# Kernel tuning notes

Hardware: AMD Instinct MI355X
Metric: run time of the kernel (lower is better)

Reference implementation:

```python
import jax, jax.numpy as jnp
import numpy as np

N = 50000
E = 625000
D = 128

def setup_inputs() -> dict:
    key = jax.random.key(0)
    ks = jax.random.split(key, 8)
    scale = 1.0 / np.sqrt(D)
    return {
        "x": jax.random.normal(ks[0], (N, D), dtype=jnp.float32),
        "edge_index": jax.random.randint(ks[1], (2, E), 0, N, dtype=jnp.int64),
        "W1_l": jax.random.normal(ks[2], (D, D), dtype=jnp.float32) * scale,
        "b1_l": jnp.zeros((D,), dtype=jnp.float32),
        "W1_r": jax.random.normal(ks[3], (D, D), dtype=jnp.float32) * scale,
        "W2_l": jax.random.normal(ks[4], (D, D), dtype=jnp.float32) * scale,
        "b2_l": jnp.zeros((D,), dtype=jnp.float32),
        "W2_r": jax.random.normal(ks[5], (D, D), dtype=jnp.float32) * scale,
    }

def _sage_conv(x, edge_index, W_l, b_l, W_r):
    # PyG SAGEConv: out = lin_l(mean_{j in N(i)} x_j) + lin_r(x_i)
    src, dst = edge_index[0], edge_index[1]
    n = x.shape[0]
    msg = x[src]                                              # [E, D] gather
    summed = jax.ops.segment_sum(msg, dst, num_segments=n)    # [N, D] scatter-add
    cnt = jax.ops.segment_sum(jnp.ones((src.shape[0],), x.dtype), dst, num_segments=n)
    mean = summed / jnp.maximum(cnt, 1.0)[:, None]            # zero in-degree -> 0
    return mean @ W_l.T + b_l + x @ W_r.T

def reference(x, edge_index, W1_l, b1_l, W1_r, W2_l, b2_l, W2_r):
    h = _sage_conv(x, edge_index, W1_l, b1_l, W1_r)
    h = jax.nn.relu(h)
    # dropout is identity in eval mode
    out = _sage_conv(h, edge_index, W2_l, b2_l, W2_r)
    return out
```

## Files before the change

kernel.cpp:

```cpp
#include <hip/hip_runtime.h>

#define D 128
#define CAP 64
#define MPAD 136
#define NBIN 196
#define BINCAP 4096
#define EPB 4096

typedef __attribute__((ext_vector_type(8))) short bf16x8;
typedef __attribute__((ext_vector_type(4))) float f32x4v;
typedef __attribute__((ext_vector_type(8))) unsigned short ushort8v;

__device__ __forceinline__ unsigned short f2b(float f) {
    unsigned int u = __float_as_uint(f);
    unsigned int r = (u + 0x7FFFu + ((u >> 16) & 1u)) >> 16;
    return (unsigned short)r;
}
__device__ __forceinline__ float b2f(unsigned short s) {
    return __uint_as_float(((unsigned int)s) << 16);
}


__global__ __launch_bounds__(256)
void prep(const float* __restrict__ x, ushort* __restrict__ xb, int n4,
          const float* __restrict__ a, const float* __restrict__ b,
          const float* __restrict__ c, const float* __restrict__ d,
          ushort* __restrict__ oa, ushort* __restrict__ ob,
          ushort* __restrict__ oc, ushort* __restrict__ od,
          int* __restrict__ ccur, ushort* __restrict__ hb, int n) {
    int i = blockIdx.x * blockDim.x + threadIdx.x;
    if (i < n4) {
        float4 v = ((const float4*)x)[i];
        ushort4 o;
        o.x = f2b(v.x); o.y = f2b(v.y); o.z = f2b(v.z); o.w = f2b(v.w);
        ((ushort4*)xb)[i] = o;
    }
    if (i < 16384) {
        int which = i >> 12, j = i & 4095;
        const float* s = which == 0 ? a : which == 1 ? b : which == 2 ? c : d;
        ushort* o = which == 0 ? oa : which == 1 ? ob : which == 2 ? oc : od;
        float4 v = ((const float4*)s)[j];
        ushort4 u;
        u.x = f2b(v.x); u.y = f2b(v.y); u.z = f2b(v.z); u.w = f2b(v.w);
        ((ushort4*)o)[j] = u;
    }
    if (i < NBIN) ccur[i] = 0;
    if (i < D) { xb[(size_t)n * D + i] = 0; hb[(size_t)n * D + i] = 0; }
}


__global__ __launch_bounds__(256)
void coarse_bin(const int* __restrict__ src, const int* __restrict__ dst, int E,
                int* __restrict__ ccur, unsigned int* __restrict__ packed) {
    __shared__ int hist[256];
    __shared__ int base[256];
    const int t = threadIdx.x;
    hist[t] = 0;
    __syncthreads();
    const int e0 = blockIdx.x * EPB;
    int mybin[16];
    int myrank[16];
    unsigned int myval[16];
#pragma unroll
    for (int k = 0; k < 16; ++k) {
        int e = e0 + k * 256 + t;
        mybin[k] = -1;
        if (e < E) {
            int dd = dst[e];
            int ss = src[e];
            int bb = dd >> 8;
            mybin[k] = bb;
            myval[k] = (unsigned int)ss | ((unsigned int)dd << 16);
            myrank[k] = atomicAdd(&hist[bb], 1);
        }
    }
    __syncthreads();
    if (t < NBIN && hist[t] > 0) base[t] = atomicAdd(&ccur[t], hist[t]);
    __syncthreads();
#pragma unroll
    for (int k = 0; k < 16; ++k) {
        if (mybin[k] >= 0) {
            int pos = base[mybin[k]] + myrank[k];
            if (pos < BINCAP) packed[(size_t)mybin[k] * BINCAP + pos] = myval[k];
        }
    }
}


__global__ __launch_bounds__(256)
void fine_csr(const unsigned int* __restrict__ packed, const int* __restrict__ ccur,
              unsigned short* __restrict__ csr, int* __restrict__ cnt, int n) {
    __shared__ int fh[256];
    const int b = blockIdx.x;
    const int t = threadIdx.x;
    fh[t] = 0;
    __syncthreads();
    int cb = min(ccur[b], BINCAP);
    const unsigned int* __restrict__ seg = packed + (size_t)b * BINCAP;
    for (int e = t; e < cb; e += 256) {
        unsigned int v = seg[e];
        int dd = (int)(v >> 16);
        int ss = (int)(v & 0xffffu);
        int r = atomicAdd(&fh[dd & 255], 1);
        if (r < CAP) csr[(size_t)dd * CAP + r] = (unsigned short)ss;
    }
    __syncthreads();
    int node = b * 256 + t;
    if (node < n) cnt[node] = fh[t];
}


template <int LAYER2>
__global__ __launch_bounds__(512, 2)
void sage_fused(const ushort* __restrict__ feat,
                const unsigned short* __restrict__ csr, const int* __restrict__ cnt,
                const ushort* __restrict__ Wl, const ushort* __restrict__ Wr,
                const float* __restrict__ bias, void* __restrict__ outp, int n) {
    __shared__ ushort Ms[128 * MPAD];
    __shared__ ushort As[128 * 32];
    __shared__ ushort Bs[128 * 32];
    const int tid = threadIdx.x;
    const int node0 = blockIdx.x * 128;

    {
        const int wv = tid >> 6;
        const int quad = (tid >> 4) & 3;
        const int l16 = tid & 15;
        const size_t co = (size_t)l16 * 8;
#pragma unroll 1
        for (int it = 0; it < 4; ++it) {
            int local = it * 32 + wv * 4 + quad;
            int node = node0 + local;
            float a0 = 0.f, a1 = 0.f, a2 = 0.f, a3 = 0.f, a4 = 0.f, a5 = 0.f, a6 = 0.f, a7 = 0.f;
            float b0 = 0.f, b1 = 0.f, b2 = 0.f, b3 = 0.f, b4 = 0.f, b5 = 0.f, b6 = 0.f, b7 = 0.f;
            float ic = 0.f;
            if (node < n) {
                int c = min(cnt[node], CAP);
                ic = 1.0f / (float)max(c, 1);
                const unsigned short* __restrict__ seg = csr + (size_t)node * CAP;
#pragma unroll 1
                for (int e = 0; e < c; e += 8) {
                    ushort8v s8 = *(const ushort8v*)&seg[e];
                    int i0 = (e + 0 < c) ? (int)s8[0] : n;
                    int i1 = (e + 1 < c) ? (int)s8[1] : n;
                    int i2 = (e + 2 < c) ? (int)s8[2] : n;
                    int i3 = (e + 3 < c) ? (int)s8[3] : n;
                    int i4 = (e + 4 < c) ? (int)s8[4] : n;
                    int i5 = (e + 5 < c) ? (int)s8[5] : n;
                    int i6 = (e + 6 < c) ? (int)s8[6] : n;
                    int i7 = (e + 7 < c) ? (int)s8[7] : n;
                    ushort8v v0 = *(const ushort8v*)&feat[(size_t)i0 * D + co];
                    ushort8v v1 = *(const ushort8v*)&feat[(size_t)i1 * D + co];
                    ushort8v v2 = *(const ushort8v*)&feat[(size_t)i2 * D + co];
                    ushort8v v3 = *(const ushort8v*)&feat[(size_t)i3 * D + co];
                    ushort8v v4 = *(const ushort8v*)&feat[(size_t)i4 * D + co];
                    ushort8v v5 = *(const ushort8v*)&feat[(size_t)i5 * D + co];
                    ushort8v v6 = *(const ushort8v*)&feat[(size_t)i6 * D + co];
                    ushort8v v7 = *(const ushort8v*)&feat[(size_t)i7 * D + co];
                    a0 += b2f(v0[0]); a1 += b2f(v0[1]); a2 += b2f(v0[2]); a3 += b2f(v0[3]);
                    a4 += b2f(v0[4]); a5 += b2f(v0[5]); a6 += b2f(v0[6]); a7 += b2f(v0[7]);
                    b0 += b2f(v1[0]); b1 += b2f(v1[1]); b2 += b2f(v1[2]); b3 += b2f(v1[3]);
                    b4 += b2f(v1[4]); b5 += b2f(v1[5]); b6 += b2f(v1[6]); b7 += b2f(v1[7]);
                    a0 += b2f(v2[0]); a1 += b2f(v2[1]); a2 += b2f(v2[2]); a3 += b2f(v2[3]);
                    a4 += b2f(v2[4]); a5 += b2f(v2[5]); a6 += b2f(v2[6]); a7 += b2f(v2[7]);
                    b0 += b2f(v3[0]); b1 += b2f(v3[1]); b2 += b2f(v3[2]); b3 += b2f(v3[3]);
                    b4 += b2f(v3[4]); b5 += b2f(v3[5]); b6 += b2f(v3[6]); b7 += b2f(v3[7]);
                    a0 += b2f(v4[0]); a1 += b2f(v4[1]); a2 += b2f(v4[2]); a3 += b2f(v4[3]);
                    a4 += b2f(v4[4]); a5 += b2f(v4[5]); a6 += b2f(v4[6]); a7 += b2f(v4[7]);
                    b0 += b2f(v5[0]); b1 += b2f(v5[1]); b2 += b2f(v5[2]); b3 += b2f(v5[3]);
                    b4 += b2f(v5[4]); b5 += b2f(v5[5]); b6 += b2f(v5[6]); b7 += b2f(v5[7]);
                    a0 += b2f(v6[0]); a1 += b2f(v6[1]); a2 += b2f(v6[2]); a3 += b2f(v6[3]);
                    a4 += b2f(v6[4]); a5 += b2f(v6[5]); a6 += b2f(v6[6]); a7 += b2f(v6[7]);
                    b0 += b2f(v7[0]); b1 += b2f(v7[1]); b2 += b2f(v7[2]); b3 += b2f(v7[3]);
                    b4 += b2f(v7[4]); b5 += b2f(v7[5]); b6 += b2f(v7[6]); b7 += b2f(v7[7]);
                }
            }
            ushort8v o;
            o[0] = f2b((a0 + b0) * ic); o[1] = f2b((a1 + b1) * ic);
            o[2] = f2b((a2 + b2) * ic); o[3] = f2b((a3 + b3) * ic);
            o[4] = f2b((a4 + b4) * ic); o[5] = f2b((a5 + b5) * ic);
            o[6] = f2b((a6 + b6) * ic); o[7] = f2b((a7 + b7) * ic);
            *(ushort8v*)&Ms[(size_t)local * MPAD + co] = o;
        }
    }
    __syncthreads();

    const int nmax = n - 1;
    const int wid = tid >> 6, l = tid & 63;
    const int wr = wid >> 2;
    const int wc = wid & 3;
    const int lrow = l & 15;
    const int lke = (l >> 4) * 8;

    f32x4v acc[4][2] = {};

#pragma unroll 1
    for (int kt = 0; kt < 4; ++kt) {
        const int ka = kt * 32;
        __syncthreads();
        {
            int row = tid >> 2;
            int kelem = ka + (tid & 3) * 8;
            __builtin_amdgcn_global_load_lds(
                (const __attribute__((address_space(1))) unsigned int*)(Wl + (size_t)row * D + kelem),
                (__attribute__((address_space(3))) unsigned int*)&Bs[tid * 8], 16, 0, 0);
        }
        __syncthreads();

        bf16x8 af[4], bf[2];
#pragma unroll
        for (int m = 0; m < 4; ++m)
            af[m] = *(const bf16x8*)&Ms[(size_t)(wr * 64 + m * 16 + lrow) * MPAD + ka + lke];
#pragma unroll
        for (int nn = 0; nn < 2; ++nn)
            bf[nn] = *(const bf16x8*)&Bs[(wc * 32 + nn * 16 + lrow) * 32 + lke];
#pragma unroll
        for (int m = 0; m < 4; ++m)
#pragma unroll
            for (int nn = 0; nn < 2; ++nn)
                acc[m][nn] = __builtin_amdgcn_mfma_f32_16x16x32_bf16(af[m], bf[nn], acc[m][nn], 0, 0, 0);
    }

#pragma unroll 1
    for (int kt = 0; kt < 4; ++kt) {
        const int ka = kt * 32;
        __syncthreads();
        {
            int row = tid >> 2;
            int kelem = ka + (tid & 3) * 8;
            int node = node0 + row; if (node > nmax) node = nmax;
            __builtin_amdgcn_global_load_lds(
                (const __attribute__((address_space(1))) unsigned int*)(feat + (size_t)node * D + kelem),
                (__attribute__((address_space(3))) unsigned int*)&As[tid * 8], 16, 0, 0);
            __builtin_amdgcn_global_load_lds(
                (const __attribute__((address_space(1))) unsigned int*)(Wr + (size_t)row * D + kelem),
                (__attribute__((address_space(3))) unsigned int*)&Bs[tid * 8], 16, 0, 0);
        }
        __syncthreads();

        bf16x8 af[4], bf[2];
#pragma unroll
        for (int m = 0; m < 4; ++m)
            af[m] = *(const bf16x8*)&As[(wr * 64 + m * 16 + lrow) * 32 + lke];
#pragma unroll
        for (int nn = 0; nn < 2; ++nn)
            bf[nn] = *(const bf16x8*)&Bs[(wc * 32 + nn * 16 + lrow) * 32 + lke];
#pragma unroll
        for (int m = 0; m < 4; ++m)
#pragma unroll
            for (int nn = 0; nn < 2; ++nn)
                acc[m][nn] = __builtin_amdgcn_mfma_f32_16x16x32_bf16(af[m], bf[nn], acc[m][nn], 0, 0, 0);
    }

    const int col = l & 15;
    const int r4 = (l >> 4) * 4;
#pragma unroll
    for (int m = 0; m < 4; ++m) {
#pragma unroll
        for (int j = 0; j < 4; ++j) {
            int node = node0 + wr * 64 + m * 16 + r4 + j;
            if (node >= n) continue;
#pragma unroll
            for (int nn = 0; nn < 2; ++nn) {
                int o = wc * 32 + nn * 16 + col;
                float v = acc[m][nn][j] + bias[o];
                if (!LAYER2) {
                    v = fmaxf(v, 0.f);
                    ((ushort*)outp)[(size_t)node * D + o] = f2b(v);
                } else {
                    ((float*)outp)[(size_t)node * D + o] = v;
                }
            }
        }
    }
}


extern "C" void kernel_launch(void* const* d_in, const int* in_sizes, int n_in,
                              void* d_out, int out_size, void* d_ws, size_t ws_size,
                              hipStream_t stream) {
    const float* x  = (const float*)d_in[0];
    const int* edge = (const int*)d_in[1];
    const float* W1l = (const float*)d_in[2];
    const float* b1  = (const float*)d_in[3];
    const float* W1r = (const float*)d_in[4];
    const float* W2l = (const float*)d_in[5];
    const float* b2  = (const float*)d_in[6];
    const float* W2r = (const float*)d_in[7];
    float* out = (float*)d_out;

    int n = in_sizes[0] / D;
    int E = in_sizes[1] / 2;
    const int* src = edge;
    const int* dst = edge + E;

    char* w = (char*)d_ws;
    auto alloc = [&](size_t bytes) {
        char* p = w;
        w += (bytes + 255) & ~(size_t)255;
        return p;
    };
    int* cnt      = (int*)alloc((size_t)n * 4);
    int* ccur     = (int*)alloc((size_t)NBIN * 4);
    unsigned int* packed = (unsigned int*)alloc((size_t)NBIN * BINCAP * 4);
    unsigned short* csr = (unsigned short*)alloc((size_t)n * CAP * 2);
    ushort* xb    = (ushort*)alloc((size_t)(n + 1) * D * 2);
    ushort* hb    = (ushort*)alloc((size_t)(n + 1) * D * 2);
    ushort* w1l   = (ushort*)alloc((size_t)D * D * 2);
    ushort* w1r   = (ushort*)alloc((size_t)D * D * 2);
    ushort* w2l   = (ushort*)alloc((size_t)D * D * 2);
    ushort* w2r   = (ushort*)alloc((size_t)D * D * 2);

    int n4 = n * D / 4;
    prep<<<(n4 + 255) / 256, 256, 0, stream>>>(x, xb, n4, W1l, W1r, W2l, W2r,
                                               w1l, w1r, w2l, w2r, ccur, hb, n);
    coarse_bin<<<(E + EPB - 1) / EPB, 256, 0, stream>>>(src, dst, E, ccur, packed);
    fine_csr<<<NBIN, 256, 0, stream>>>(packed, ccur, csr, cnt, n);

    int blocks = (n + 127) / 128;
    sage_fused<0><<<blocks, 512, 0, stream>>>(xb, csr, cnt, w1l, w1r, b1, hb, n);
    sage_fused<1><<<blocks, 512, 0, stream>>>(hb, csr, cnt, w2l, w2r, b2, out, n);
}
```

Baseline: 95.59 us.

## Halve node tile to 64 and read GEMM operands directly from global

Shrinks each fused SAGE block from 128 to 64 nodes, doubling the grid and cutting shared memory to the aggregation buffer alone. The weight and self-feature operands for the MFMA loops are now loaded straight from global memory into registers instead of being staged through LDS, which removes the per-k-tile barriers and LDS round trips. In exchange, weights are re-read by every block from cache, and each weight tile is reused by fewer rows.

```diff
diff --git a/kernel.cpp b/kernel.cpp
--- a/kernel.cpp
+++ b/kernel.cpp
@@ -6,6 +6,7 @@
 #define NBIN 196
 #define BINCAP 4096
 #define EPB 4096
+#define TN 64
 
 typedef __attribute__((ext_vector_type(8))) short bf16x8;
 typedef __attribute__((ext_vector_type(4))) float f32x4v;
@@ -116,11 +117,9 @@
                 const unsigned short* __restrict__ csr, const int* __restrict__ cnt,
                 const ushort* __restrict__ Wl, const ushort* __restrict__ Wr,
                 const float* __restrict__ bias, void* __restrict__ outp, int n) {
-    __shared__ ushort Ms[128 * MPAD];
-    __shared__ ushort As[128 * 32];
-    __shared__ ushort Bs[128 * 32];
+    __shared__ ushort Ms[TN * MPAD];
     const int tid = threadIdx.x;
-    const int node0 = blockIdx.x * 128;
+    const int node0 = blockIdx.x * TN;
 
     {
         const int wv = tid >> 6;
@@ -128,7 +127,7 @@
         const int l16 = tid & 15;
         const size_t co = (size_t)l16 * 8;
 #pragma unroll 1
-        for (int it = 0; it < 4; ++it) {
+        for (int it = 0; it < 2; ++it) {
             int local = it * 32 + wv * 4 + quad;
             int node = node0 + local;
             float a0 = 0.f, a1 = 0.f, a2 = 0.f, a3 = 0.f, a4 = 0.f, a5 = 0.f, a6 = 0.f, a7 = 0.f;
@@ -192,61 +191,39 @@
     const int lrow = l & 15;
     const int lke = (l >> 4) * 8;
 
-    f32x4v acc[4][2] = {};
-
-#pragma unroll 1
+    f32x4v acc[2][2] = {};
+
+#pragma unroll 2
     for (int kt = 0; kt < 4; ++kt) {
         const int ka = kt * 32;
-        __syncthreads();
-        {
-            int row = tid >> 2;
-            int kelem = ka + (tid & 3) * 8;
-            __builtin_amdgcn_global_load_lds(
-                (const __attribute__((address_space(1))) unsigned int*)(Wl + (size_t)row * D + kelem),
-                (__attribute__((address_space(3))) unsigned int*)&Bs[tid * 8], 16, 0, 0);
-        }
-        __syncthreads();
-
-        bf16x8 af[4], bf[2];
-#pragma unroll
-        for (int m = 0; m < 4; ++m)
-            af[m] = *(const bf16x8*)&Ms[(size_t)(wr * 64 + m * 16 + lrow) * MPAD + ka + lke];
+        bf16x8 af[2], bf[2];
+#pragma unroll
+        for (int m = 0; m < 2; ++m)
+            af[m] = *(const bf16x8*)&Ms[(size_t)(wr * 32 + m * 16 + lrow) * MPAD + ka + lke];
 #pragma unroll
         for (int nn = 0; nn < 2; ++nn)
-            bf[nn] = *(const bf16x8*)&Bs[(wc * 32 + nn * 16 + lrow) * 32 + lke];
-#pragma unroll
-        for (int m = 0; m < 4; ++m)
+            bf[nn] = *(const bf16x8*)&Wl[(size_t)(wc * 32 + nn * 16 + lrow) * D + ka + lke];
+#pragma unroll
+        for (int m = 0; m < 2; ++m)
 #pragma unroll
             for (int nn = 0; nn < 2; ++nn)
                 acc[m][nn] = __builtin_amdgcn_mfma_f32_16x16x32_bf16(af[m], bf[nn], acc[m][nn], 0, 0, 0);
     }
 
-#pragma unroll 1
+#pragma unroll 2
     for (int kt = 0; kt < 4; ++kt) {
         const int ka = kt * 32;
-        __syncthreads();
-        {
-            int row = tid >> 2;
-            int kelem = ka + (tid & 3) * 8;
-            int node = node0 + row; if (node > nmax) node = nmax;
-            __builtin_amdgcn_global_load_lds(
-                (const __attribute__((address_space(1))) unsigned int*)(feat + (size_t)node * D + kelem),
-                (__attribute__((address_space(3))) unsigned int*)&As[tid * 8], 16, 0, 0);
-            __builtin_amdgcn_global_load_lds(
-                (const __attribute__((address_space(1))) unsigned int*)(Wr + (size_t)row * D + kelem),
-                (__attribute__((address_space(3))) unsigned int*)&Bs[tid * 8], 16, 0, 0);
-        }
-        __syncthreads();
-
-        bf16x8 af[4], bf[2];
-#pragma unroll
-        for (int m = 0; m < 4; ++m)
-            af[m] = *(const bf16x8*)&As[(wr * 64 + m * 16 + lrow) * 32 + lke];
+        bf16x8 af[2], bf[2];
+#pragma unroll
+        for (int m = 0; m < 2; ++m) {
+            int node = node0 + wr * 32 + m * 16 + lrow; if (node > nmax) node = nmax;
+            af[m] = *(const bf16x8*)&feat[(size_t)node * D + ka + lke];
+        }
 #pragma unroll
         for (int nn = 0; nn < 2; ++nn)
-            bf[nn] = *(const bf16x8*)&Bs[(wc * 32 + nn * 16 + lrow) * 32 + lke];
-#pragma unroll
-        for (int m = 0; m < 4; ++m)
+            bf[nn] = *(const bf16x8*)&Wr[(size_t)(wc * 32 + nn * 16 + lrow) * D + ka + lke];
+#pragma unroll
+        for (int m = 0; m < 2; ++m)
 #pragma unroll
             for (int nn = 0; nn < 2; ++nn)
                 acc[m][nn] = __builtin_amdgcn_mfma_f32_16x16x32_bf16(af[m], bf[nn], acc[m][nn], 0, 0, 0);
@@ -255,10 +232,10 @@
     const int col = l & 15;
     const int r4 = (l >> 4) * 4;
 #pragma unroll
-    for (int m = 0; m < 4; ++m) {
+    for (int m = 0; m < 2; ++m) {
 #pragma unroll
         for (int j = 0; j < 4; ++j) {
-            int node = node0 + wr * 64 + m * 16 + r4 + j;
+            int node = node0 + wr * 32 + m * 16 + r4 + j;
             if (node >= n) continue;
 #pragma unroll
             for (int nn = 0; nn < 2; ++nn) {
@@ -317,7 +294,7 @@
     coarse_bin<<<(E + EPB - 1) / EPB, 256, 0, stream>>>(src, dst, E, ccur, packed);
     fine_csr<<<NBIN, 256, 0, stream>>>(packed, ccur, csr, cnt, n);
 
-    int blocks = (n + 127) / 128;
+    int blocks = (n + TN - 1) / TN;
     sage_fused<0><<<blocks, 512, 0, stream>>>(xb, csr, cnt, w1l, w1r, b1, hb, n);
     sage_fused<1><<<blocks, 512, 0, stream>>>(hb, csr, cnt, w2l, w2r, b2, out, n);
 }
```

New measurement: 127.7 us. 33.6% more time.
